# Optimization experiments

Hardware: AMD Instinct MI355X
Metric: run time of the kernel (lower is better)

## Reference

```python
import jax, jax.numpy as jnp
import numpy as np

EPS = 1e-5  # torch nn.LayerNorm default eps


def layer_norm(x, w, b):
    mu = jnp.mean(x, axis=-1, keepdims=True)
    var = jnp.mean(jnp.square(x - mu), axis=-1, keepdims=True)
    return (x - mu) * jax.lax.rsqrt(var + EPS) * w + b


def setup_inputs() -> dict:
    key = jax.random.key(0)
    k1, k2 = jax.random.split(key)
    B, T, D, N = 8, 1024, 512, 8192
    x = jax.random.normal(k1, (B, T, D), dtype=jnp.float32)
    ln_weight = jnp.ones((D,), dtype=jnp.float32)
    ln_bias = jnp.zeros((D,), dtype=jnp.float32)
    embd = jax.random.normal(k2, (N, D), dtype=jnp.float32)
    return {"x": x, "ln_weight": ln_weight, "ln_bias": ln_bias, "embd": embd}


def reference(x, ln_weight, ln_bias, embd):
    # LayerNorm
    h = layer_norm(x, ln_weight, ln_bias)            # [B, T, D]
    # codebook logits + argmax select
    logits = jnp.einsum("btd,nd->btn", h, embd)      # [B, T, N]
    idxs = jnp.argmax(logits, axis=-1)               # [B, T]
    q1 = embd[idxs]                                  # [B, T, D] gather
    # straight-through combine
    q2 = h + jax.lax.stop_gradient(q1 - h)
    quantize = (q1 + q2) / 2
    return quantize, idxs
```

## Files before the change

### kernel.cpp

```cpp
#include <hip/hip_runtime.h>
#include <hip/hip_bf16.h>

#define ROWS   8192
#define DIM    512
#define NCODES 8192
#define BM     128
#define CGW    1024
#define NNT    8
#define NKT    8
#define MARGIN 3.0f

using i32x4 = __attribute__((ext_vector_type(4))) int;
typedef unsigned char u8;

__device__ __forceinline__ void gload_lds16(const void* g, void* l) {
    __builtin_amdgcn_global_load_lds((const __attribute__((address_space(1))) void*)g,
                                     (__attribute__((address_space(3))) void*)l,
                                     16, 0, 0);
}

__device__ __forceinline__ unsigned int pack4(int a, int b, int c, int d) {
    return (a & 255) | ((b & 255) << 8) | ((c & 255) << 16) | ((unsigned)(d & 255) << 24);
}

__global__ __launch_bounds__(256) void prep_kernel(
    const float* __restrict__ x, const float* __restrict__ lw,
    const float* __restrict__ lb, const float* __restrict__ embd,
    float2* __restrict__ stats, float* __restrict__ sh, float* __restrict__ se,
    u8* __restrict__ Hq, u8* __restrict__ Eq)
{
    __shared__ float red[4];
    const int w    = threadIdx.x >> 6;
    const int lane = threadIdx.x & 63;
    const int b    = blockIdx.x;

    if (b < 2048) {
        const int row = b * 4 + w;
        const float* xr = x + (size_t)row * DIM + lane * 8;
        float4 v0 = *(const float4*)(xr);
        float4 v1 = *(const float4*)(xr + 4);
        float s = (v0.x + v0.y) + (v0.z + v0.w) + (v1.x + v1.y) + (v1.z + v1.w);
        float q = v0.x*v0.x + v0.y*v0.y + v0.z*v0.z + v0.w*v0.w
                + v1.x*v1.x + v1.y*v1.y + v1.z*v1.z + v1.w*v1.w;
        #pragma unroll
        for (int off = 1; off < 64; off <<= 1) {
            s += __shfl_xor(s, off);
            q += __shfl_xor(q, off);
        }
        float mu   = s * (1.0f / DIM);
        float var  = q * (1.0f / DIM) - mu * mu;
        float rstd = rsqrtf(var + 1e-5f);
        if (lane == 0) stats[row] = make_float2(mu, rstd);

        float4 w0 = *(const float4*)(lw + lane * 8);
        float4 w1 = *(const float4*)(lw + lane * 8 + 4);
        float4 b0 = *(const float4*)(lb + lane * 8);
        float4 b1 = *(const float4*)(lb + lane * 8 + 4);
        float hv[8] = {
            (v0.x - mu) * rstd * w0.x + b0.x, (v0.y - mu) * rstd * w0.y + b0.y,
            (v0.z - mu) * rstd * w0.z + b0.z, (v0.w - mu) * rstd * w0.w + b0.w,
            (v1.x - mu) * rstd * w1.x + b1.x, (v1.y - mu) * rstd * w1.y + b1.y,
            (v1.z - mu) * rstd * w1.z + b1.z, (v1.w - mu) * rstd * w1.w + b1.w };

        float am = 0.0f;
        #pragma unroll
        for (int j = 0; j < 8; ++j) am = fmaxf(am, fabsf(hv[j]));
        #pragma unroll
        for (int off = 1; off < 64; off <<= 1) am = fmaxf(am, __shfl_xor(am, off));
        const float inv = (am > 0.0f) ? (127.0f / am) : 0.0f;
        if (lane == 0) sh[row] = am * (1.0f / 127.0f);

        int qi[8];
        #pragma unroll
        for (int j = 0; j < 8; ++j) qi[j] = __float2int_rn(hv[j] * inv);
        uint2 p = make_uint2(pack4(qi[0], qi[1], qi[2], qi[3]),
                             pack4(qi[4], qi[5], qi[6], qi[7]));
        *(uint2*)(Hq + (size_t)row * DIM + lane * 8) = p;
    } else {
        const int chunk = b - 2048;
        const int row   = chunk * 64 + (threadIdx.x >> 2);
        const int off0  = (threadIdx.x & 3) * 128;
        const float* er = embd + (size_t)row * DIM + off0;

        float4 v[32];
        float am = 0.0f;
        #pragma unroll
        for (int j = 0; j < 32; ++j) {
            v[j] = *(const float4*)(er + j * 4);
            am = fmaxf(am, fmaxf(fmaxf(fabsf(v[j].x), fabsf(v[j].y)),
                                 fmaxf(fabsf(v[j].z), fabsf(v[j].w))));
        }
        #pragma unroll
        for (int off = 1; off < 64; off <<= 1) am = fmaxf(am, __shfl_xor(am, off));
        if (lane == 0) red[w] = am;
        __syncthreads();
        am = fmaxf(fmaxf(red[0], red[1]), fmaxf(red[2], red[3]));

        const float inv = (am > 0.0f) ? (127.0f / am) : 0.0f;
        if (threadIdx.x == 0) se[chunk] = am * (1.0f / 127.0f);

        u8* out = Eq + (size_t)row * DIM + off0;
        #pragma unroll
        for (int j = 0; j < 32; j += 4) {
            uint4 o;
            o.x = pack4(__float2int_rn(v[j+0].x*inv), __float2int_rn(v[j+0].y*inv),
                        __float2int_rn(v[j+0].z*inv), __float2int_rn(v[j+0].w*inv));
            o.y = pack4(__float2int_rn(v[j+1].x*inv), __float2int_rn(v[j+1].y*inv),
                        __float2int_rn(v[j+1].z*inv), __float2int_rn(v[j+1].w*inv));
            o.z = pack4(__float2int_rn(v[j+2].x*inv), __float2int_rn(v[j+2].y*inv),
                        __float2int_rn(v[j+2].z*inv), __float2int_rn(v[j+2].w*inv));
            o.w = pack4(__float2int_rn(v[j+3].x*inv), __float2int_rn(v[j+3].y*inv),
                        __float2int_rn(v[j+3].z*inv), __float2int_rn(v[j+3].w*inv));
            *(uint4*)(out + j * 4) = o;
        }
    }
}

__global__ __launch_bounds__(256, 2) void gemm_argmax_kernel(
    const u8* __restrict__ Hq, const u8* __restrict__ Eq,
    const float* __restrict__ sh, const float* __restrict__ se,
    float* __restrict__ pval, int* __restrict__ pidx)
{
    __shared__ __align__(16) u8 Apan[BM * DIM];
    __shared__ __align__(16) u8 Bs[2][128 * 64];

    const int tid  = threadIdx.x;
    const int w    = tid >> 6;
    const int lane = tid & 63;
    const int r_   = lane & 15;
    const int g    = lane >> 4;
    const int wr   = w >> 1;
    const int wc   = w & 1;

    const int bid  = blockIdx.x;
    const int colg = bid & 7;
    const int rowp = bid >> 3;
    const int r0   = rowp * BM;
    const int c0   = colg * CGW;

    #pragma unroll
    for (int jj = 0; jj < 16; ++jj) {
        const int j    = w * 16 + jj;
        const int drow = j * 2 + (lane >> 5);
        const int dcol = (lane & 31) * 16;
        gload_lds16(Hq + (size_t)(r0 + drow) * DIM + (dcol ^ ((drow & 7) << 4)),
                    &Apan[j * 1024]);
    }

    const int db0 = (w * 2 + 0) * 16 + (lane >> 2);
    const int db1 = (w * 2 + 1) * 16 + (lane >> 2);
    const int lc  = (lane & 3) * 16;
    const u8* sB0 = Eq + (size_t)(c0 + db0) * DIM + (lc ^ (((db0 >> 1) & 3) << 4));
    const u8* sB1 = Eq + (size_t)(c0 + db1) * DIM + (lc ^ (((db1 >> 1) & 3) << 4));
    const int ub0 = (w * 2 + 0) * 1024, ub1 = (w * 2 + 1) * 1024;

    const int fldA = (r_ & 7) << 4;
    const int ab   = (wr * 64 + r_) * 512;
    const int bb   = (wc * 64 + r_) * 64 + ((g * 16) ^ (((r_ >> 1) & 3) << 4));

#define STAGE_B(NT2, KT2, SL) do {                                      \
        const size_t off_ = (size_t)(NT2) * (128 * DIM) + (KT2) * 64;   \
        gload_lds16(sB0 + off_, &Bs[SL][ub0]);                          \
        gload_lds16(sB1 + off_, &Bs[SL][ub1]);                          \
    } while (0)
#define MF(M, N, AV, BV) \
        acc[M][N] = __builtin_amdgcn_mfma_i32_16x16x64_i8(AV, BV, acc[M][N], 0, 0, 0)

    STAGE_B(0, 0, 0);

    for (int nt = 0; nt < NNT; ++nt) {
        i32x4 acc[4][4];
        #pragma unroll
        for (int m = 0; m < 4; ++m)
            #pragma unroll
            for (int n = 0; n < 4; ++n) acc[m][n] = (i32x4){0, 0, 0, 0};

        #pragma unroll
        for (int kt = 0; kt < NKT; ++kt) {
            if (kt < 7) {
                STAGE_B(nt, kt + 1, (kt + 1) & 1);
                asm volatile("s_waitcnt vmcnt(2)" ::: "memory");
            } else if (nt < 7) {
                STAGE_B(nt + 1, 0, 0);
                asm volatile("s_waitcnt vmcnt(2)" ::: "memory");
            } else {
                asm volatile("s_waitcnt vmcnt(0)" ::: "memory");
            }
            __builtin_amdgcn_s_barrier();

            const int ak = (kt * 64 + g * 16) ^ fldA;
            i32x4 a0 = *(const i32x4*)&Apan[ab + 0 * 8192 + ak];
            i32x4 a1 = *(const i32x4*)&Apan[ab + 1 * 8192 + ak];
            i32x4 a2 = *(const i32x4*)&Apan[ab + 2 * 8192 + ak];
            i32x4 a3 = *(const i32x4*)&Apan[ab + 3 * 8192 + ak];
            const u8* Bp = &Bs[kt & 1][0];
            i32x4 b0 = *(const i32x4*)(Bp + bb + 0 * 1024);
            i32x4 b1 = *(const i32x4*)(Bp + bb + 1 * 1024);
            i32x4 b2 = *(const i32x4*)(Bp + bb + 2 * 1024);
            i32x4 b3 = *(const i32x4*)(Bp + bb + 3 * 1024);

            __builtin_amdgcn_s_setprio(1);
            MF(0, 0, a0, b0); MF(0, 1, a0, b1); MF(0, 2, a0, b2); MF(0, 3, a0, b3);
            MF(1, 0, a1, b0); MF(1, 1, a1, b1); MF(1, 2, a1, b2); MF(1, 3, a1, b3);
            MF(2, 0, a2, b0); MF(2, 1, a2, b1); MF(2, 2, a2, b2); MF(2, 3, a2, b3);
            MF(3, 0, a3, b0); MF(3, 1, a3, b1); MF(3, 2, a3, b2); MF(3, 3, a3, b3);
            __builtin_amdgcn_s_setprio(0);

            __builtin_amdgcn_s_barrier();
        }

        const int chunk = colg * 16 + nt * 2 + wc;
        const int cb    = chunk * 64;
        const float se_ch = se[chunk];
        #pragma unroll
        for (int m = 0; m < 4; ++m) {
            #pragma unroll
            for (int reg = 0; reg < 4; ++reg) {
                int ka = (acc[m][0][reg] << 7) | (63 - r_);
                int kb = (acc[m][1][reg] << 7) | (47 - r_);
                int kc = (acc[m][2][reg] << 7) | (31 - r_);
                int kd = (acc[m][3][reg] << 7) | (15 - r_);
                int m1 = max(ka, kb), n1 = min(ka, kb);
                int m2 = max(kc, kd), n2 = min(kc, kd);
                int k1 = max(m1, m2);
                int k2 = max(min(m1, m2), max(n1, n2));
                #pragma unroll
                for (int off = 1; off < 16; off <<= 1) {
                    int o1 = __shfl_xor(k1, off);
                    int o2 = __shfl_xor(k2, off);
                    k2 = max(max(k2, o2), min(k1, o1));
                    k1 = max(k1, o1);
                }
                if (r_ == 0) {
                    const int row = r0 + wr * 64 + m * 16 + g * 4 + reg;
                    const float sc = sh[row];
                    const size_t base = (size_t)row * 256 + chunk * 2;
                    pval[base]     = (float)(k1 >> 7) * (sc * se_ch);
                    pval[base + 1] = (float)(k2 >> 7) * (sc * se_ch);
                    pidx[base]     = cb + 63 - (k1 & 63);
                    pidx[base + 1] = cb + 63 - (k2 & 63);
                }
            }
        }
    }

#undef MF
#undef STAGE_B
}

__global__ __launch_bounds__(256) void finalize_kernel(
    const float* __restrict__ x, const float* __restrict__ lw,
    const float* __restrict__ lb, const float* __restrict__ embd,
    const float2* __restrict__ stats,
    const float* __restrict__ pval, const int* __restrict__ pidx,
    float* __restrict__ outq, float* __restrict__ outi)
{
    const int w    = threadIdx.x >> 6;
    const int lane = threadIdx.x & 63;
    const int row  = blockIdx.x * 4 + w;

    const float4 cv = *(const float4*)&pval[(size_t)row * 256 + lane * 4];
    const int4   ci = *(const int4*)  &pidx[(size_t)row * 256 + lane * 4];
    float vv[4] = { cv.x, cv.y, cv.z, cv.w };
    int   ii[4] = { ci.x, ci.y, ci.z, ci.w };

    float M = fmaxf(fmaxf(vv[0], vv[1]), fmaxf(vv[2], vv[3]));
    #pragma unroll
    for (int off = 1; off < 64; off <<= 1) M = fmaxf(M, __shfl_xor(M, off));
    const float T = M - MARGIN;

    const float2 st = stats[row];
    const float mu = st.x, rstd = st.y;
    const float* xr = x + (size_t)row * DIM + lane * 8;
    float4 x0 = *(const float4*)(xr);
    float4 x1 = *(const float4*)(xr + 4);
    float4 w0 = *(const float4*)(lw + lane * 8);
    float4 w1 = *(const float4*)(lw + lane * 8 + 4);
    float4 b0 = *(const float4*)(lb + lane * 8);
    float4 b1 = *(const float4*)(lb + lane * 8 + 4);
    float h[8] = {
        (x0.x - mu) * rstd * w0.x + b0.x, (x0.y - mu) * rstd * w0.y + b0.y,
        (x0.z - mu) * rstd * w0.z + b0.z, (x0.w - mu) * rstd * w0.w + b0.w,
        (x1.x - mu) * rstd * w1.x + b1.x, (x1.y - mu) * rstd * w1.y + b1.y,
        (x1.z - mu) * rstd * w1.z + b1.z, (x1.w - mu) * rstd * w1.w + b1.w };

    float bestv = -3.4e38f; int besti = 0x7fffffff;
    #pragma unroll
    for (int s = 0; s < 4; ++s) {
        unsigned long long msk = __ballot(vv[s] >= T);
        while (msk) {
            const int L = __ffsll(msk) - 1;
            msk &= msk - 1;
            const int cand = __shfl(ii[s], L);
            const float* er = embd + (size_t)cand * DIM + lane * 8;
            float4 e0 = *(const float4*)er;
            float4 e1 = *(const float4*)(er + 4);
            float d = h[0]*e0.x + h[1]*e0.y + h[2]*e0.z + h[3]*e0.w
                    + h[4]*e1.x + h[5]*e1.y + h[6]*e1.z + h[7]*e1.w;
            #pragma unroll
            for (int off = 1; off < 64; off <<= 1) d += __shfl_xor(d, off);
            if (d > bestv || (d == bestv && cand < besti)) { bestv = d; besti = cand; }
        }
    }

    const float* er = embd + (size_t)besti * DIM + lane * 8;
    float4 q0 = *(const float4*)er;
    float4 q1 = *(const float4*)(er + 4);
    float* qr = outq + (size_t)row * DIM + lane * 8;
    *(float4*)(qr)     = q0;
    *(float4*)(qr + 4) = q1;
    if (lane == 0) outi[row] = (float)besti;
}

extern "C" void kernel_launch(void* const* d_in, const int* in_sizes, int n_in,
                              void* d_out, int out_size, void* d_ws, size_t ws_size,
                              hipStream_t stream) {
    const float* x    = (const float*)d_in[0];
    const float* lnw  = (const float*)d_in[1];
    const float* lnb  = (const float*)d_in[2];
    const float* embd = (const float*)d_in[3];

    float* outq = (float*)d_out;
    float* outi = outq + (size_t)ROWS * DIM;

    char* ws = (char*)d_ws;
    float2* stats = (float2*)ws;
    float*  sh    = (float*)(ws + (1 << 16));
    float*  se    = (float*)(ws + (1 << 16) + (1 << 15));
    u8*     Hq    = (u8*)(ws + (1 << 17));
    u8*     Eq    = (u8*)(ws + (1 << 17) + (4 << 20));
    float*  pval  = (float*)(ws + (1 << 17) + (8 << 20));
    int*    pidx  = (int*)  (ws + (1 << 17) + (16 << 20));

    prep_kernel<<<2176, 256, 0, stream>>>(x, lnw, lnb, embd, stats, sh, se, Hq, Eq);

    gemm_argmax_kernel<<<512, 256, 0, stream>>>(Hq, Eq, sh, se, pval, pidx);

    finalize_kernel<<<ROWS / 4, 256, 0, stream>>>(x, lnw, lnb, embd, stats,
                                                  pval, pidx, outq, outi);
}
```

Before: 114.3 us.

## Keep A fragments in registers and stage full-K codebook tiles in LDS

The int8 GEMM+argmax kernel now uses 512-thread blocks covering 512 rows by 512 codes. Each wave holds its 64-row A panel (full K) in registers instead of in LDS. The B tiles (128 codes by full K) are double-buffered in LDS, so there is one barrier per 128-code tile rather than two per 64-wide K step. This cuts barrier and sync overhead and A-side LDS traffic, at the cost of many more VGPRs, 128KB of LDS per block, and half as many blocks, which lowers occupancy and raises the risk of poor latency hiding.

```diff
diff --git a/kernel.cpp b/kernel.cpp
--- a/kernel.cpp
+++ b/kernel.cpp
@@ -4,10 +4,6 @@
 #define ROWS   8192
 #define DIM    512
 #define NCODES 8192
-#define BM     128
-#define CGW    1024
-#define NNT    8
-#define NKT    8
 #define MARGIN 3.0f
 
 using i32x4 = __attribute__((ext_vector_type(4))) int;
@@ -116,131 +112,128 @@
     }
 }
 
-__global__ __launch_bounds__(256, 2) void gemm_argmax_kernel(
+__global__ __launch_bounds__(512, 2) void gemm_argmax_kernel(
     const u8* __restrict__ Hq, const u8* __restrict__ Eq,
     const float* __restrict__ sh, const float* __restrict__ se,
     float* __restrict__ pval, int* __restrict__ pidx)
 {
-    __shared__ __align__(16) u8 Apan[BM * DIM];
-    __shared__ __align__(16) u8 Bs[2][128 * 64];
+    __shared__ __align__(16) u8 Bs[2][128 * DIM];
 
     const int tid  = threadIdx.x;
     const int w    = tid >> 6;
     const int lane = tid & 63;
     const int r_   = lane & 15;
     const int g    = lane >> 4;
-    const int wr   = w >> 1;
-    const int wc   = w & 1;
 
     const int bid  = blockIdx.x;
-    const int colg = bid & 7;
-    const int rowp = bid >> 3;
-    const int r0   = rowp * BM;
-    const int c0   = colg * CGW;
-
+    const int colg = ((bid & 7) << 1) | ((bid >> 3) & 1);
+    const int rowp = bid >> 4;
+    const int r0   = rowp * 512;
+    const int c0   = colg * 512;
+
+    const u8* Abase = Hq + (size_t)(r0 + w * 64 + r_) * DIM + g * 16;
+    i32x4 af[4][8];
     #pragma unroll
-    for (int jj = 0; jj < 16; ++jj) {
-        const int j    = w * 16 + jj;
-        const int drow = j * 2 + (lane >> 5);
-        const int dcol = (lane & 31) * 16;
-        gload_lds16(Hq + (size_t)(r0 + drow) * DIM + (dcol ^ ((drow & 7) << 4)),
-                    &Apan[j * 1024]);
-    }
-
-    const int db0 = (w * 2 + 0) * 16 + (lane >> 2);
-    const int db1 = (w * 2 + 1) * 16 + (lane >> 2);
-    const int lc  = (lane & 3) * 16;
-    const u8* sB0 = Eq + (size_t)(c0 + db0) * DIM + (lc ^ (((db0 >> 1) & 3) << 4));
-    const u8* sB1 = Eq + (size_t)(c0 + db1) * DIM + (lc ^ (((db1 >> 1) & 3) << 4));
-    const int ub0 = (w * 2 + 0) * 1024, ub1 = (w * 2 + 1) * 1024;
-
-    const int fldA = (r_ & 7) << 4;
-    const int ab   = (wr * 64 + r_) * 512;
-    const int bb   = (wc * 64 + r_) * 64 + ((g * 16) ^ (((r_ >> 1) & 3) << 4));
-
-#define STAGE_B(NT2, KT2, SL) do {                                      \
-        const size_t off_ = (size_t)(NT2) * (128 * DIM) + (KT2) * 64;   \
-        gload_lds16(sB0 + off_, &Bs[SL][ub0]);                          \
-        gload_lds16(sB1 + off_, &Bs[SL][ub1]);                          \
+    for (int m = 0; m < 4; ++m)
+        #pragma unroll
+        for (int kt = 0; kt < 8; ++kt)
+            af[m][kt] = *(const i32x4*)(Abase + (size_t)m * 16 * DIM + kt * 64);
+
+    const int sdrow = (tid >> 5) & 1 ? 0 : 0; (void)sdrow;
+    const int drow_lo = tid >> 5;
+    const int dk      = (tid & 31) * 16;
+    const u8* sB = Eq + (size_t)(c0 + drow_lo) * DIM;
+    const int ub = tid * 16;
+
+#define STAGE_B(NT, SL) do {                                              \
+        _Pragma("unroll")                                                 \
+        for (int j = 0; j < 8; ++j) {                                     \
+            const int drow = j * 16 + drow_lo;                            \
+            gload_lds16(sB + ((size_t)(NT) * 128 + j * 16) * DIM          \
+                           + (dk ^ ((drow & 7) << 4)),                    \
+                        &Bs[SL][j * 8192 + ub]);                          \
+        }                                                                 \
     } while (0)
 #define MF(M, N, AV, BV) \
         acc[M][N] = __builtin_amdgcn_mfma_i32_16x16x64_i8(AV, BV, acc[M][N], 0, 0, 0)
 
-    STAGE_B(0, 0, 0);
-
-    for (int nt = 0; nt < NNT; ++nt) {
-        i32x4 acc[4][4];
-        #pragma unroll
-        for (int m = 0; m < 4; ++m)
+    STAGE_B(0, 0);
+    asm volatile("s_waitcnt vmcnt(0)" ::: "memory");
+    __builtin_amdgcn_s_barrier();
+
+    const int fldB = (r_ & 7) << 4;
+
+    for (int nt = 0; nt < 4; ++nt) {
+        const u8* Bp = &Bs[nt & 1][0];
+        if (nt < 3) STAGE_B(nt + 1, (nt + 1) & 1);
+
+        #pragma unroll
+        for (int ch = 0; ch < 2; ++ch) {
+            i32x4 acc[4][4];
             #pragma unroll
-            for (int n = 0; n < 4; ++n) acc[m][n] = (i32x4){0, 0, 0, 0};
-
-        #pragma unroll
-        for (int kt = 0; kt < NKT; ++kt) {
-            if (kt < 7) {
-                STAGE_B(nt, kt + 1, (kt + 1) & 1);
-                asm volatile("s_waitcnt vmcnt(2)" ::: "memory");
-            } else if (nt < 7) {
-                STAGE_B(nt + 1, 0, 0);
-                asm volatile("s_waitcnt vmcnt(2)" ::: "memory");
-            } else {
-                asm volatile("s_waitcnt vmcnt(0)" ::: "memory");
+            for (int m = 0; m < 4; ++m)
+                #pragma unroll
+                for (int n = 0; n < 4; ++n) acc[m][n] = (i32x4){0, 0, 0, 0};
+
+            const int bb = (ch * 64 + r_) * 512;
+
+            #pragma unroll
+            for (int kt = 0; kt < 8; ++kt) {
+                const int ko = (kt * 64 + g * 16) ^ fldB;
+                i32x4 b0 = *(const i32x4*)(Bp + bb + 0 * 8192 + ko);
+                i32x4 b1 = *(const i32x4*)(Bp + bb + 1 * 8192 + ko);
+                i32x4 b2 = *(const i32x4*)(Bp + bb + 2 * 8192 + ko);
+                i32x4 b3 = *(const i32x4*)(Bp + bb + 3 * 8192 + ko);
+                __builtin_amdgcn_s_setprio(1);
+                MF(0, 0, af[0][kt], b0); MF(0, 1, af[0][kt], b1);
+                MF(0, 2, af[0][kt], b2); MF(0, 3, af[0][kt], b3);
+                MF(1, 0, af[1][kt], b0); MF(1, 1, af[1][kt], b1);
+                MF(1, 2, af[1][kt], b2); MF(1, 3, af[1][kt], b3);
+                MF(2, 0, af[2][kt], b0); MF(2, 1, af[2][kt], b1);
+                MF(2, 2, af[2][kt], b2); MF(2, 3, af[2][kt], b3);
+                MF(3, 0, af[3][kt], b0); MF(3, 1, af[3][kt], b1);
+                MF(3, 2, af[3][kt], b2); MF(3, 3, af[3][kt], b3);
+                __builtin_amdgcn_s_setprio(0);
             }
-            __builtin_amdgcn_s_barrier();
-
-            const int ak = (kt * 64 + g * 16) ^ fldA;
-            i32x4 a0 = *(const i32x4*)&Apan[ab + 0 * 8192 + ak];
-            i32x4 a1 = *(const i32x4*)&Apan[ab + 1 * 8192 + ak];
-            i32x4 a2 = *(const i32x4*)&Apan[ab + 2 * 8192 + ak];
-            i32x4 a3 = *(const i32x4*)&Apan[ab + 3 * 8192 + ak];
-            const u8* Bp = &Bs[kt & 1][0];
-            i32x4 b0 = *(const i32x4*)(Bp + bb + 0 * 1024);
-            i32x4 b1 = *(const i32x4*)(Bp + bb + 1 * 1024);
-            i32x4 b2 = *(const i32x4*)(Bp + bb + 2 * 1024);
-            i32x4 b3 = *(const i32x4*)(Bp + bb + 3 * 1024);
-
-            __builtin_amdgcn_s_setprio(1);
-            MF(0, 0, a0, b0); MF(0, 1, a0, b1); MF(0, 2, a0, b2); MF(0, 3, a0, b3);
-            MF(1, 0, a1, b0); MF(1, 1, a1, b1); MF(1, 2, a1, b2); MF(1, 3, a1, b3);
-            MF(2, 0, a2, b0); MF(2, 1, a2, b1); MF(2, 2, a2, b2); MF(2, 3, a2, b3);
-            MF(3, 0, a3, b0); MF(3, 1, a3, b1); MF(3, 2, a3, b2); MF(3, 3, a3, b3);
-            __builtin_amdgcn_s_setprio(0);
-
-            __builtin_amdgcn_s_barrier();
-        }
-
-        const int chunk = colg * 16 + nt * 2 + wc;
-        const int cb    = chunk * 64;
-        const float se_ch = se[chunk];
-        #pragma unroll
-        for (int m = 0; m < 4; ++m) {
+
+            const int chunk = colg * 8 + nt * 2 + ch;
+            const int cb    = chunk * 64;
+            const float se_ch = se[chunk];
             #pragma unroll
-            for (int reg = 0; reg < 4; ++reg) {
-                int ka = (acc[m][0][reg] << 7) | (63 - r_);
-                int kb = (acc[m][1][reg] << 7) | (47 - r_);
-                int kc = (acc[m][2][reg] << 7) | (31 - r_);
-                int kd = (acc[m][3][reg] << 7) | (15 - r_);
-                int m1 = max(ka, kb), n1 = min(ka, kb);
-                int m2 = max(kc, kd), n2 = min(kc, kd);
-                int k1 = max(m1, m2);
-                int k2 = max(min(m1, m2), max(n1, n2));
+            for (int m = 0; m < 4; ++m) {
                 #pragma unroll
-                for (int off = 1; off < 16; off <<= 1) {
-                    int o1 = __shfl_xor(k1, off);
-                    int o2 = __shfl_xor(k2, off);
-                    k2 = max(max(k2, o2), min(k1, o1));
-                    k1 = max(k1, o1);
-                }
-                if (r_ == 0) {
-                    const int row = r0 + wr * 64 + m * 16 + g * 4 + reg;
-                    const float sc = sh[row];
-                    const size_t base = (size_t)row * 256 + chunk * 2;
-                    pval[base]     = (float)(k1 >> 7) * (sc * se_ch);
-                    pval[base + 1] = (float)(k2 >> 7) * (sc * se_ch);
-                    pidx[base]     = cb + 63 - (k1 & 63);
-                    pidx[base + 1] = cb + 63 - (k2 & 63);
+                for (int reg = 0; reg < 4; ++reg) {
+                    int ka = (acc[m][0][reg] << 7) | (63 - r_);
+                    int kb = (acc[m][1][reg] << 7) | (47 - r_);
+                    int kc = (acc[m][2][reg] << 7) | (31 - r_);
+                    int kd = (acc[m][3][reg] << 7) | (15 - r_);
+                    int m1 = max(ka, kb), n1 = min(ka, kb);
+                    int m2 = max(kc, kd), n2 = min(kc, kd);
+                    int k1 = max(m1, m2);
+                    int k2 = max(min(m1, m2), max(n1, n2));
+                    #pragma unroll
+                    for (int off = 1; off < 16; off <<= 1) {
+                        int o1 = __shfl_xor(k1, off);
+                        int o2 = __shfl_xor(k2, off);
+                        k2 = max(max(k2, o2), min(k1, o1));
+                        k1 = max(k1, o1);
+                    }
+                    if (r_ == 0) {
+                        const int row = r0 + w * 64 + m * 16 + g * 4 + reg;
+                        const float sc = sh[row];
+                        const size_t base = (size_t)row * 256 + chunk * 2;
+                        pval[base]     = (float)(k1 >> 7) * (sc * se_ch);
+                        pval[base + 1] = (float)(k2 >> 7) * (sc * se_ch);
+                        pidx[base]     = cb + 63 - (k1 & 63);
+                        pidx[base + 1] = cb + 63 - (k2 & 63);
+                    }
                 }
             }
+        }
+
+        if (nt < 3) {
+            asm volatile("s_waitcnt vmcnt(0)" ::: "memory");
+            __builtin_amdgcn_s_barrier();
         }
     }
 
@@ -334,7 +327,7 @@
 
     prep_kernel<<<2176, 256, 0, stream>>>(x, lnw, lnb, embd, stats, sh, se, Hq, Eq);
 
-    gemm_argmax_kernel<<<512, 256, 0, stream>>>(Hq, Eq, sh, se, pval, pidx);
+    gemm_argmax_kernel<<<256, 512, 0, stream>>>(Hq, Eq, sh, se, pval, pidx);
 
     finalize_kernel<<<ROWS / 4, 256, 0, stream>>>(x, lnw, lnb, embd, stats,
                                                   pval, pidx, outq, outi);
```

Measured after the change: 135.6 us. +18.7%, slower.
